# Performance work log

Hardware: AMD Instinct MI355X
Metric: run time of the kernel (lower is better)

The kernel has to match this reference:

```python
import jax, jax.numpy as jnp
import numpy as np

B, S, D, H, DH = 2, 2048, 1024, 16, 64
SCALE = float(np.sqrt(DH))
IGNORE = -100000.0


def setup_inputs() -> dict:
    key = jax.random.key(0)
    ks = jax.random.split(key, 9)
    s = 0.02
    return {
        "x": jax.random.normal(ks[0], (B, S, D), dtype=jnp.float32),
        "W_Q": jax.random.normal(ks[1], (H, DH, D), dtype=jnp.float32) * s,
        "W_K": jax.random.normal(ks[2], (H, DH, D), dtype=jnp.float32) * s,
        "W_V": jax.random.normal(ks[3], (H, DH, D), dtype=jnp.float32) * s,
        "W_O": jax.random.normal(ks[4], (H, D, DH), dtype=jnp.float32) * s,
        "b_Q": jax.random.normal(ks[5], (H, DH), dtype=jnp.float32) * s,
        "b_K": jax.random.normal(ks[6], (H, DH), dtype=jnp.float32) * s,
        "b_V": jax.random.normal(ks[7], (H, DH), dtype=jnp.float32) * s,
        "b_O": jax.random.normal(ks[8], (D,), dtype=jnp.float32) * s,
        "mask": jnp.tril(jnp.ones((S, S), dtype=bool)),  # causal, global attn_type
    }


def reference(x, W_Q, W_K, W_V, W_O, b_Q, b_K, b_V, b_O, mask):
    # q,k,v: [batch, pos, head, d_head]
    q = jnp.einsum('ihm,bpm->bpih', W_Q, x) + b_Q
    k = jnp.einsum('ihm,bpm->bpih', W_K, x) + b_K
    v = jnp.einsum('ihm,bpm->bpih', W_V, x) + b_V
    # scores: [batch, head, q_pos, k_pos]
    attn_scores = jnp.einsum('bpih,bqih->bipq', q, k) / SCALE
    attn_scores = jnp.where(mask, attn_scores, IGNORE)
    attn = jax.nn.softmax(attn_scores, axis=-1)
    # z: [batch, q_pos, head, d_head]
    z = jnp.einsum('bpih,biqp->bqih', v, attn)
    out = jnp.einsum('idh,bqih->bqd', W_O, z) + b_O
    return out
```

## Files before the change

### kernel.cpp

```cpp
#include <hip/hip_runtime.h>
#include <stdint.h>

typedef __attribute__((ext_vector_type(8))) short bf16x8;
typedef __attribute__((ext_vector_type(4))) float f32x4;
typedef __attribute__((ext_vector_type(16))) float f32x16;
typedef __attribute__((ext_vector_type(4))) unsigned short us4;

#define LOG2E 1.44269504088896340736f

__device__ __forceinline__ unsigned short f2bf(float f) {
    union { float f; unsigned u; } v; v.f = f;
    unsigned r = v.u + 0x7FFFu + ((v.u >> 16) & 1u);
    return (unsigned short)(r >> 16);
}
__device__ __forceinline__ float bf2f(unsigned short u) {
    return __uint_as_float(((unsigned)u) << 16);
}

__device__ __forceinline__ unsigned cvtpk(float lo, float hi) {
    unsigned r;
    asm("v_cvt_pk_bf16_f32 %0, %1, %2" : "=v"(r) : "v"(lo), "v"(hi));
    return r;
}
__device__ __forceinline__ void plswap(unsigned &a, unsigned &b) {
    asm volatile("v_permlane32_swap_b32 %0, %1" : "+v"(a), "+v"(b));
}

__device__ __forceinline__ void gld16(const void* g, void* l) {
    __builtin_amdgcn_global_load_lds((const __attribute__((address_space(1))) void*)g,
                                     (__attribute__((address_space(3))) void*)l, 16, 0, 0);
}

__global__ void k_cvt_all(
    const float* __restrict__ x,  const float* __restrict__ WQ,
    const float* __restrict__ WK, const float* __restrict__ WV,
    const float* __restrict__ WO,
    unsigned short* __restrict__ xb,  unsigned short* __restrict__ wqb,
    unsigned short* __restrict__ wkb, unsigned short* __restrict__ wvb,
    unsigned short* __restrict__ wob)
{
    const int blk = blockIdx.x;
    if (blk < 7168) {
        const float* in; unsigned short* out; int base;
        if (blk < 4096)      { in = x;  out = xb;  base = blk; }
        else if (blk < 5120) { in = WQ; out = wqb; base = blk - 4096; }
        else if (blk < 6144) { in = WK; out = wkb; base = blk - 5120; }
        else                 { in = WV; out = wvb; base = blk - 6144; }
        int i = base * 256 + threadIdx.x;
        float4 v = ((const float4*)in)[i];
        us4 o; o.x = f2bf(v.x); o.y = f2bf(v.y); o.z = f2bf(v.z); o.w = f2bf(v.w);
        *(us4*)(out + (size_t)i * 4) = o;
    } else {
        int t = (blk - 7168) * 256 + threadIdx.x;
        int d = t >> 10, nn = t & 1023, i = nn >> 6, h = nn & 63;
        wob[t] = f2bf(WO[(((size_t)i << 10) + d) * 64 + h]);
    }
}

__global__ __launch_bounds__(256) void k_gemm_qkv(
    const unsigned short* __restrict__ Xb,
    const unsigned short* __restrict__ Wq, const unsigned short* __restrict__ Wk,
    const unsigned short* __restrict__ Wv,
    const float* __restrict__ bQ, const float* __restrict__ bK, const float* __restrict__ bV,
    unsigned short* __restrict__ Qb, unsigned short* __restrict__ Kb, unsigned short* __restrict__ VTb)
{
    __shared__ unsigned short As[128][128];
    __shared__ unsigned short Bs[64][128];
    const int which = blockIdx.z;
    const unsigned short* Wp = which == 0 ? Wq : (which == 1 ? Wk : Wv);
    const int bm = blockIdx.x, bn = blockIdx.y;
    const int t = threadIdx.x, lane = t & 63, w = t >> 6;
    const int l15 = lane & 15, l4 = lane >> 4;
    const int rsw = l15 & 7;
    const int c0 = w * 64 + lane;
    const int arow = bm << 7, brow = bn << 6;
    f32x4 acc[2][4] = {};

    for (int k0 = 0; k0 < 1024; k0 += 128) {
        #pragma unroll
        for (int it = 0; it < 8; ++it) {
            int c = it * 256 + c0;
            int row = c >> 4, sl = (c & 15) ^ (row & 7);
            gld16(Xb + ((size_t)(arow + row)) * 1024 + k0 + sl * 8, (char*)As + (c << 4));
        }
        #pragma unroll
        for (int it = 0; it < 4; ++it) {
            int c = it * 256 + c0;
            int row = c >> 4, sl = (c & 15) ^ (row & 7);
            gld16(Wp + ((size_t)(brow + row)) * 1024 + k0 + sl * 8, (char*)Bs + (c << 4));
        }
        __syncthreads();
        const char* Ab = (const char*)As;
        const char* Bb = (const char*)Bs;
        #pragma unroll
        for (int kk = 0; kk < 4; ++kk) {
            bf16x8 af[2], bfg[4];
            #pragma unroll
            for (int m = 0; m < 2; ++m)
                af[m] = *(const bf16x8*)(Ab + (w * 32 + m * 16 + l15) * 256 + (((kk * 4 + l4) ^ rsw) << 4));
            #pragma unroll
            for (int n = 0; n < 4; ++n)
                bfg[n] = *(const bf16x8*)(Bb + (n * 16 + l15) * 256 + (((kk * 4 + l4) ^ rsw) << 4));
            __builtin_amdgcn_s_setprio(1);
            #pragma unroll
            for (int m = 0; m < 2; ++m)
                #pragma unroll
                for (int n = 0; n < 4; ++n)
                    acc[m][n] = __builtin_amdgcn_mfma_f32_16x16x32_bf16(af[m], bfg[n], acc[m][n], 0, 0, 0);
            __builtin_amdgcn_s_setprio(0);
        }
        __syncthreads();
    }
    #pragma unroll
    for (int m = 0; m < 2; ++m) {
        #pragma unroll
        for (int n = 0; n < 4; ++n) {
            int col = (bn << 6) + n * 16 + l15;
            int i = col >> 6, h = col & 63;
            float bias = which == 0 ? bQ[col] : (which == 1 ? bK[col] : bV[col]);
            #pragma unroll
            for (int r = 0; r < 4; ++r) {
                int p = (bm << 7) + w * 32 + m * 16 + (l4 << 2) + r;
                int b = p >> 11, s = p & 2047;
                float v = acc[m][n][r] + bias;
                if (which == 0)
                    Qb[(((((size_t)b << 4) + i) << 11) + s) * 64 + h] = f2bf(v * (0.125f * LOG2E));
                else if (which == 1)
                    Kb[(((((size_t)b << 4) + i) << 11) + s) * 64 + h] = f2bf(v);
                else
                    VTb[(((((size_t)b << 4) + i) << 6) + h) * 2048 + s] = f2bf(v);
            }
        }
    }
}

__global__ __launch_bounds__(128) void k_attn(
    const unsigned short* __restrict__ Qb, const unsigned short* __restrict__ Kb,
    const unsigned short* __restrict__ VTb,
    unsigned short* __restrict__ Zp, float* __restrict__ Lse)
{
    __shared__ __align__(16) char Lbuf[16384];
    const int id = (int)blockIdx.x;
    const int bi = id & 31;
    const int r = id >> 5;
    const int c = 31 - (r >> 1);
    const int part = r & 1;
    const int n = c + 1, n0 = (n + 1) >> 1;
    const int t0 = part ? n0 : 0, t1 = part ? n : n0;
    const int lane = threadIdx.x & 63, w = threadIdx.x >> 6;
    const int l31 = lane & 31, hi = lane >> 5;
    const unsigned short* Qh = Qb + (size_t)bi * 2048 * 64;
    const char* Khb = (const char*)(Kb + (size_t)bi * 2048 * 64);
    const char* Vhb = (const char*)(VTb + (size_t)bi * 64 * 2048);
    const int q0 = c * 64 + w * 32;
    const int q = q0 + l31;

    bf16x8 qf[4];
    #pragma unroll
    for (int kk = 0; kk < 4; ++kk)
        qf[kk] = *(const bf16x8*)&Qh[(size_t)q * 64 + kk * 16 + hi * 8];

    const int r8 = lane >> 3;
    const int swz = ((lane & 7) * 16) ^ (r8 << 4);
    const int koff = r8 * 128 + swz;
    const int voff = r8 * 4096 + swz;

    const int rsw = (l31 & 7) << 4;
    int kaddr[8];
    #pragma unroll
    for (int i = 0; i < 8; ++i)
        kaddr[i] = (l31 + 32 * (i >> 2)) * 128 + ((32 * (i & 3) + 16 * hi) ^ rsw);
    int vcol[4];
    #pragma unroll
    for (int f = 0; f < 4; ++f)
        vcol[f] = ((f * 32 + 16 * hi) ^ rsw);

    f32x16 za0 = {}, za1 = {};
    float m_run = -1e30f, l_run = 0.f;

    if (t0 < t1) {
        if (w == 0) {
            const char* src = Khb + (size_t)t0 * 8192 + koff;
            #pragma unroll
            for (int it = 0; it < 8; ++it) gld16(src + it * 1024, &Lbuf[0] + it * 1024);
        } else {
            const char* src = Vhb + (size_t)t0 * 128 + voff;
            #pragma unroll
            for (int it = 0; it < 8; ++it) gld16(src + it * 32768, &Lbuf[8192] + it * 1024);
        }
    }

    for (int t = t0; t < t1; ++t) {
        __syncthreads();
        const char* KL = &Lbuf[0];
        const char* VL = &Lbuf[8192];
        bf16x8 ka[8];
        #pragma unroll
        for (int i = 0; i < 8; ++i) ka[i] = *(const bf16x8*)(KL + kaddr[i]);
        bf16x8 vf0[4], vf1[4];
        #pragma unroll
        for (int f = 0; f < 4; ++f) {
            vf0[f] = *(const bf16x8*)(VL + l31 * 128 + vcol[f]);
            vf1[f] = *(const bf16x8*)(VL + (l31 + 32) * 128 + vcol[f]);
        }
        __syncthreads();
        if (t + 1 < t1) {
            if (w == 0) {
                const char* src = Khb + (size_t)(t + 1) * 8192 + koff;
                #pragma unroll
                for (int it = 0; it < 8; ++it) gld16(src + it * 1024, &Lbuf[0] + it * 1024);
            } else {
                const char* src = Vhb + (size_t)(t + 1) * 128 + voff;
                #pragma unroll
                for (int it = 0; it < 8; ++it) gld16(src + it * 32768, &Lbuf[8192] + it * 1024);
            }
        }

        const bool full = !(t == c && w == 0);
        f32x16 s0 = {}, s1;
        __builtin_amdgcn_s_setprio(1);
        #pragma unroll
        for (int kk = 0; kk < 4; ++kk)
            s0 = __builtin_amdgcn_mfma_f32_32x32x16_bf16(ka[kk], qf[kk], s0, 0, 0, 0);
        if (full) {
            f32x16 z = {};
            #pragma unroll
            for (int kk = 0; kk < 4; ++kk)
                z = __builtin_amdgcn_mfma_f32_32x32x16_bf16(ka[4 + kk], qf[kk], z, 0, 0, 0);
            s1 = z;
        }
        __builtin_amdgcn_s_setprio(0);

        if (!full) {
            #pragma unroll
            for (int j = 0; j < 16; ++j) s1[j] = -100000.0f;
        }
        if (t == c) {
            #pragma unroll
            for (int j = 0; j < 16; ++j) {
                int kv0 = (j & 3) + 8 * (j >> 2) + 4 * hi;
                if (c * 64 + kv0 > q) s0[j] = -100000.0f;
                if (c * 64 + kv0 + 32 > q) s1[j] = -100000.0f;
            }
        }
        float tmax = -1e30f;
        #pragma unroll
        for (int j = 0; j < 16; ++j) tmax = fmaxf(tmax, fmaxf(s0[j], s1[j]));
        tmax = fmaxf(tmax, __shfl_xor(tmax, 32, 64));
        if (!__all(tmax <= m_run + 8.0f)) {
            float newm = fmaxf(m_run, tmax);
            float alpha = exp2f(m_run - newm);
            m_run = newm;
            l_run *= alpha;
            za0 *= alpha; za1 *= alpha;
        }
        float rsum = 0.f;
        #pragma unroll
        for (int j = 0; j < 16; ++j) { s0[j] = exp2f(s0[j] - m_run); rsum += s0[j]; }
        if (full) {
            #pragma unroll
            for (int j = 0; j < 16; ++j) { s1[j] = exp2f(s1[j] - m_run); rsum += s1[j]; }
        }
        rsum += __shfl_xor(rsum, 32, 64);
        l_run += rsum;

        union { unsigned u[4]; bf16x8 v; } pk0, pk1, pk2, pk3;
        {
            unsigned a0 = cvtpk(s0[0], s0[1]),  a1 = cvtpk(s0[2], s0[3]);
            unsigned a2 = cvtpk(s0[4], s0[5]),  a3 = cvtpk(s0[6], s0[7]);
            plswap(a0, a2); plswap(a1, a3);
            pk0.u[0] = a0; pk0.u[1] = a1; pk0.u[2] = a2; pk0.u[3] = a3;
            unsigned b0 = cvtpk(s0[8], s0[9]),  b1 = cvtpk(s0[10], s0[11]);
            unsigned b2 = cvtpk(s0[12], s0[13]), b3 = cvtpk(s0[14], s0[15]);
            plswap(b0, b2); plswap(b1, b3);
            pk1.u[0] = b0; pk1.u[1] = b1; pk1.u[2] = b2; pk1.u[3] = b3;
        }
        if (full) {
            unsigned a0 = cvtpk(s1[0], s1[1]),  a1 = cvtpk(s1[2], s1[3]);
            unsigned a2 = cvtpk(s1[4], s1[5]),  a3 = cvtpk(s1[6], s1[7]);
            plswap(a0, a2); plswap(a1, a3);
            pk2.u[0] = a0; pk2.u[1] = a1; pk2.u[2] = a2; pk2.u[3] = a3;
            unsigned b0 = cvtpk(s1[8], s1[9]),  b1 = cvtpk(s1[10], s1[11]);
            unsigned b2 = cvtpk(s1[12], s1[13]), b3 = cvtpk(s1[14], s1[15]);
            plswap(b0, b2); plswap(b1, b3);
            pk3.u[0] = b0; pk3.u[1] = b1; pk3.u[2] = b2; pk3.u[3] = b3;
        }
        __builtin_amdgcn_s_setprio(1);
        za0 = __builtin_amdgcn_mfma_f32_32x32x16_bf16(vf0[0], pk0.v, za0, 0, 0, 0);
        za1 = __builtin_amdgcn_mfma_f32_32x32x16_bf16(vf1[0], pk0.v, za1, 0, 0, 0);
        za0 = __builtin_amdgcn_mfma_f32_32x32x16_bf16(vf0[1], pk1.v, za0, 0, 0, 0);
        za1 = __builtin_amdgcn_mfma_f32_32x32x16_bf16(vf1[1], pk1.v, za1, 0, 0, 0);
        if (full) {
            za0 = __builtin_amdgcn_mfma_f32_32x32x16_bf16(vf0[2], pk2.v, za0, 0, 0, 0);
            za1 = __builtin_amdgcn_mfma_f32_32x32x16_bf16(vf1[2], pk2.v, za1, 0, 0, 0);
            za0 = __builtin_amdgcn_mfma_f32_32x32x16_bf16(vf0[3], pk3.v, za0, 0, 0, 0);
            za1 = __builtin_amdgcn_mfma_f32_32x32x16_bf16(vf1[3], pk3.v, za1, 0, 0, 0);
        }
        __builtin_amdgcn_s_setprio(0);
    }

    const float rl = (l_run > 0.f) ? 1.0f / l_run : 0.f;
    const float lse = (l_run > 0.f) ? m_run + log2f(l_run) : -1e30f;
    const int pb = (part << 5) + bi;
    unsigned short* zp = Zp + ((size_t)pb * 2048 + q) * 64;
    #pragma unroll
    for (int nn = 0; nn < 2; ++nn) {
        #pragma unroll
        for (int gg = 0; gg < 4; ++gg) {
            int dh0 = nn * 32 + 8 * gg + 4 * hi;
            us4 o;
            float v0 = (nn ? za1[4 * gg + 0] : za0[4 * gg + 0]) * rl;
            float v1 = (nn ? za1[4 * gg + 1] : za0[4 * gg + 1]) * rl;
            float v2 = (nn ? za1[4 * gg + 2] : za0[4 * gg + 2]) * rl;
            float v3 = (nn ? za1[4 * gg + 3] : za0[4 * gg + 3]) * rl;
            o.x = f2bf(v0); o.y = f2bf(v1); o.z = f2bf(v2); o.w = f2bf(v3);
            *(us4*)(zp + dh0) = o;
        }
    }
    if (hi == 0) Lse[(size_t)pb * 2048 + q] = lse;
}

__global__ __launch_bounds__(256) void k_combine(
    const unsigned short* __restrict__ Zp, const float* __restrict__ Lse,
    unsigned short* __restrict__ Zb)
{
    const int tid = blockIdx.x * 256 + threadIdx.x;
    const int dc = tid & 7, q = (tid >> 3) & 2047, bi = tid >> 14;
    const float l0 = Lse[(size_t)bi * 2048 + q];
    const float l1 = Lse[(size_t)(32 + bi) * 2048 + q];
    const float M = fmaxf(l0, l1);
    float e0 = exp2f(l0 - M), e1 = exp2f(l1 - M);
    const float rs = 1.0f / (e0 + e1);
    e0 *= rs; e1 *= rs;
    const size_t base = ((size_t)bi * 2048 + q) * 64 + dc * 8;
    bf16x8 z0 = *(const bf16x8*)(Zp + base);
    bf16x8 z1 = *(const bf16x8*)(Zp + (size_t)32 * 2048 * 64 + base);
    const int b = bi >> 4, ih = bi & 15;
    unsigned short* op = Zb + (((size_t)b * 2048 + q) << 10) + ih * 64 + dc * 8;
    bf16x8 o;
    #pragma unroll
    for (int j = 0; j < 8; ++j) {
        float v = e0 * bf2f((unsigned short)z0[j]) + e1 * bf2f((unsigned short)z1[j]);
        o[j] = (short)f2bf(v);
    }
    *(bf16x8*)op = o;
}

__global__ __launch_bounds__(256) void k_gemm_out(
    const unsigned short* __restrict__ Zb, const unsigned short* __restrict__ Wo,
    const float* __restrict__ bO, float* __restrict__ out)
{
    __shared__ unsigned short As[128][128];
    __shared__ unsigned short Bs[64][128];
    const int bm = blockIdx.x, bn = blockIdx.y;
    const int t = threadIdx.x, lane = t & 63, w = t >> 6;
    const int l15 = lane & 15, l4 = lane >> 4;
    const int rsw = l15 & 7;
    const int c0 = w * 64 + lane;
    const int arow = bm << 7, brow = bn << 6;
    f32x4 acc[2][4] = {};

    for (int k0 = 0; k0 < 1024; k0 += 128) {
        #pragma unroll
        for (int it = 0; it < 8; ++it) {
            int c = it * 256 + c0;
            int row = c >> 4, sl = (c & 15) ^ (row & 7);
            gld16(Zb + ((size_t)(arow + row)) * 1024 + k0 + sl * 8, (char*)As + (c << 4));
        }
        #pragma unroll
        for (int it = 0; it < 4; ++it) {
            int c = it * 256 + c0;
            int row = c >> 4, sl = (c & 15) ^ (row & 7);
            gld16(Wo + ((size_t)(brow + row)) * 1024 + k0 + sl * 8, (char*)Bs + (c << 4));
        }
        __syncthreads();
        const char* Ab = (const char*)As;
        const char* Bb = (const char*)Bs;
        #pragma unroll
        for (int kk = 0; kk < 4; ++kk) {
            bf16x8 af[2], bfg[4];
            #pragma unroll
            for (int m = 0; m < 2; ++m)
                af[m] = *(const bf16x8*)(Ab + (w * 32 + m * 16 + l15) * 256 + (((kk * 4 + l4) ^ rsw) << 4));
            #pragma unroll
            for (int n = 0; n < 4; ++n)
                bfg[n] = *(const bf16x8*)(Bb + (n * 16 + l15) * 256 + (((kk * 4 + l4) ^ rsw) << 4));
            __builtin_amdgcn_s_setprio(1);
            #pragma unroll
            for (int m = 0; m < 2; ++m)
                #pragma unroll
                for (int n = 0; n < 4; ++n)
                    acc[m][n] = __builtin_amdgcn_mfma_f32_16x16x32_bf16(af[m], bfg[n], acc[m][n], 0, 0, 0);
            __builtin_amdgcn_s_setprio(0);
        }
        __syncthreads();
    }
    #pragma unroll
    for (int m = 0; m < 2; ++m) {
        #pragma unroll
        for (int n = 0; n < 4; ++n) {
            int col = (bn << 6) + n * 16 + l15;
            float bias = bO[col];
            #pragma unroll
            for (int r = 0; r < 4; ++r) {
                int p = (bm << 7) + w * 32 + m * 16 + (l4 << 2) + r;
                out[(size_t)p * 1024 + col] = acc[m][n][r] + bias;
            }
        }
    }
}

extern "C" void kernel_launch(void* const* d_in, const int* in_sizes, int n_in,
                              void* d_out, int out_size, void* d_ws, size_t ws_size,
                              hipStream_t stream)
{
    const float* x  = (const float*)d_in[0];
    const float* WQ = (const float*)d_in[1];
    const float* WK = (const float*)d_in[2];
    const float* WV = (const float*)d_in[3];
    const float* WO = (const float*)d_in[4];
    const float* bQ = (const float*)d_in[5];
    const float* bK = (const float*)d_in[6];
    const float* bV = (const float*)d_in[7];
    const float* bO = (const float*)d_in[8];
    float* out = (float*)d_out;

    char* w = (char*)d_ws;
    unsigned short* xb  = (unsigned short*)w; w += (size_t)4096 * 1024 * 2;
    unsigned short* wqb = (unsigned short*)w; w += (size_t)1024 * 1024 * 2;
    unsigned short* wkb = (unsigned short*)w; w += (size_t)1024 * 1024 * 2;
    unsigned short* wvb = (unsigned short*)w; w += (size_t)1024 * 1024 * 2;
    unsigned short* wob = (unsigned short*)w; w += (size_t)1024 * 1024 * 2;
    unsigned short* Qb  = (unsigned short*)w; w += (size_t)4096 * 1024 * 2;
    unsigned short* Kb  = (unsigned short*)w; w += (size_t)4096 * 1024 * 2;
    unsigned short* VTb = (unsigned short*)w; w += (size_t)4096 * 1024 * 2;
    unsigned short* Zb  = (unsigned short*)w; w += (size_t)4096 * 1024 * 2;
    unsigned short* Zp  = (unsigned short*)w; w += (size_t)2 * 32 * 2048 * 64 * 2;
    float*          Lse = (float*)w;          w += (size_t)2 * 32 * 2048 * 4;

    k_cvt_all<<<11264, 256, 0, stream>>>(x, WQ, WK, WV, WO, xb, wqb, wkb, wvb, wob);

    k_gemm_qkv<<<dim3(32, 16, 3), 256, 0, stream>>>(xb, wqb, wkb, wvb, bQ, bK, bV, Qb, Kb, VTb);
    k_attn<<<2048, 128, 0, stream>>>(Qb, Kb, VTb, Zp, Lse);
    k_combine<<<2048, 256, 0, stream>>>(Zp, Lse, Zb);
    k_gemm_out<<<dim3(32, 16), 256, 0, stream>>>(Zb, wob, bO, out);
}
```

Before: 125.5 us.

## Process two 32-query sub-blocks per wave to double K/V tile reuse

Each attention workgroup now handles 128 query rows: each wave owns two 32-row query sub-blocks, with separate accumulators and softmax state for each. This replaces the previous 64 rows per workgroup, and the grid shrinks from 2048 to 1024 workgroups. The key range is split evenly in two for the two partial-sum parts, and waves skip tiles beyond their causal diagonal. The aim is to halve LDS staging and global K/V traffic per query and to amortise barriers. The costs are higher register pressure, fewer workgroups, and idle waves on diagonal tiles.

```diff
diff --git a/kernel.cpp b/kernel.cpp
--- a/kernel.cpp
+++ b/kernel.cpp
@@ -142,23 +142,25 @@
     __shared__ __align__(16) char Lbuf[16384];
     const int id = (int)blockIdx.x;
     const int bi = id & 31;
-    const int r = id >> 5;
-    const int c = 31 - (r >> 1);
-    const int part = r & 1;
-    const int n = c + 1, n0 = (n + 1) >> 1;
-    const int t0 = part ? n0 : 0, t1 = part ? n : n0;
+    const int rr = id >> 5;
+    const int g = 15 - (rr >> 1);
+    const int part = rr & 1;
+    const int t0 = part * (g + 1), t1 = t0 + g + 1;
     const int lane = threadIdx.x & 63, w = threadIdx.x >> 6;
     const int l31 = lane & 31, hi = lane >> 5;
     const unsigned short* Qh = Qb + (size_t)bi * 2048 * 64;
     const char* Khb = (const char*)(Kb + (size_t)bi * 2048 * 64);
     const char* Vhb = (const char*)(VTb + (size_t)bi * 64 * 2048);
-    const int q0 = c * 64 + w * 32;
-    const int q = q0 + l31;
-
-    bf16x8 qf[4];
-    #pragma unroll
-    for (int kk = 0; kk < 4; ++kk)
-        qf[kk] = *(const bf16x8*)&Qh[(size_t)q * 64 + kk * 16 + hi * 8];
+    const int qA = g * 128 + w * 64 + l31;
+    const int qB = qA + 32;
+    const int dq = 2 * g + w;
+
+    bf16x8 qfA[4], qfB[4];
+    #pragma unroll
+    for (int kk = 0; kk < 4; ++kk) {
+        qfA[kk] = *(const bf16x8*)&Qh[(size_t)qA * 64 + kk * 16 + hi * 8];
+        qfB[kk] = *(const bf16x8*)&Qh[(size_t)qB * 64 + kk * 16 + hi * 8];
+    }
 
     const int r8 = lane >> 3;
     const int swz = ((lane & 7) * 16) ^ (r8 << 4);
@@ -175,33 +177,33 @@
     for (int f = 0; f < 4; ++f)
         vcol[f] = ((f * 32 + 16 * hi) ^ rsw);
 
-    f32x16 za0 = {}, za1 = {};
-    float m_run = -1e30f, l_run = 0.f;
-
-    if (t0 < t1) {
-        if (w == 0) {
-            const char* src = Khb + (size_t)t0 * 8192 + koff;
-            #pragma unroll
-            for (int it = 0; it < 8; ++it) gld16(src + it * 1024, &Lbuf[0] + it * 1024);
-        } else {
-            const char* src = Vhb + (size_t)t0 * 128 + voff;
-            #pragma unroll
-            for (int it = 0; it < 8; ++it) gld16(src + it * 32768, &Lbuf[8192] + it * 1024);
-        }
+    f32x16 zaA0 = {}, zaA1 = {}, zaB0 = {}, zaB1 = {};
+    float mA = -1e30f, lA = 0.f, mB = -1e30f, lB = 0.f;
+
+    if (w == 0) {
+        const char* src = Khb + (size_t)t0 * 8192 + koff;
+        #pragma unroll
+        for (int it = 0; it < 8; ++it) gld16(src + it * 1024, &Lbuf[0] + it * 1024);
+    } else {
+        const char* src = Vhb + (size_t)t0 * 128 + voff;
+        #pragma unroll
+        for (int it = 0; it < 8; ++it) gld16(src + it * 32768, &Lbuf[8192] + it * 1024);
     }
 
     for (int t = t0; t < t1; ++t) {
-        __syncthreads();
-        const char* KL = &Lbuf[0];
-        const char* VL = &Lbuf[8192];
-        bf16x8 ka[8];
-        #pragma unroll
-        for (int i = 0; i < 8; ++i) ka[i] = *(const bf16x8*)(KL + kaddr[i]);
-        bf16x8 vf0[4], vf1[4];
-        #pragma unroll
-        for (int f = 0; f < 4; ++f) {
-            vf0[f] = *(const bf16x8*)(VL + l31 * 128 + vcol[f]);
-            vf1[f] = *(const bf16x8*)(VL + (l31 + 32) * 128 + vcol[f]);
+        const bool active = (t <= dq);
+        __syncthreads();
+        bf16x8 ka[8], vf0[4], vf1[4];
+        if (active) {
+            const char* KL = &Lbuf[0];
+            const char* VL = &Lbuf[8192];
+            #pragma unroll
+            for (int i = 0; i < 8; ++i) ka[i] = *(const bf16x8*)(KL + kaddr[i]);
+            #pragma unroll
+            for (int f = 0; f < 4; ++f) {
+                vf0[f] = *(const bf16x8*)(VL + l31 * 128 + vcol[f]);
+                vf1[f] = *(const bf16x8*)(VL + (l31 + 32) * 128 + vcol[f]);
+            }
         }
         __syncthreads();
         if (t + 1 < t1) {
@@ -215,109 +217,120 @@
                 for (int it = 0; it < 8; ++it) gld16(src + it * 32768, &Lbuf[8192] + it * 1024);
             }
         }
-
-        const bool full = !(t == c && w == 0);
-        f32x16 s0 = {}, s1;
-        __builtin_amdgcn_s_setprio(1);
-        #pragma unroll
-        for (int kk = 0; kk < 4; ++kk)
-            s0 = __builtin_amdgcn_mfma_f32_32x32x16_bf16(ka[kk], qf[kk], s0, 0, 0, 0);
-        if (full) {
-            f32x16 z = {};
-            #pragma unroll
-            for (int kk = 0; kk < 4; ++kk)
-                z = __builtin_amdgcn_mfma_f32_32x32x16_bf16(ka[4 + kk], qf[kk], z, 0, 0, 0);
-            s1 = z;
-        }
-        __builtin_amdgcn_s_setprio(0);
-
-        if (!full) {
-            #pragma unroll
-            for (int j = 0; j < 16; ++j) s1[j] = -100000.0f;
-        }
-        if (t == c) {
-            #pragma unroll
-            for (int j = 0; j < 16; ++j) {
-                int kv0 = (j & 3) + 8 * (j >> 2) + 4 * hi;
-                if (c * 64 + kv0 > q) s0[j] = -100000.0f;
-                if (c * 64 + kv0 + 32 > q) s1[j] = -100000.0f;
-            }
-        }
-        float tmax = -1e30f;
-        #pragma unroll
-        for (int j = 0; j < 16; ++j) tmax = fmaxf(tmax, fmaxf(s0[j], s1[j]));
-        tmax = fmaxf(tmax, __shfl_xor(tmax, 32, 64));
-        if (!__all(tmax <= m_run + 8.0f)) {
-            float newm = fmaxf(m_run, tmax);
-            float alpha = exp2f(m_run - newm);
-            m_run = newm;
-            l_run *= alpha;
-            za0 *= alpha; za1 *= alpha;
-        }
-        float rsum = 0.f;
-        #pragma unroll
-        for (int j = 0; j < 16; ++j) { s0[j] = exp2f(s0[j] - m_run); rsum += s0[j]; }
-        if (full) {
-            #pragma unroll
-            for (int j = 0; j < 16; ++j) { s1[j] = exp2f(s1[j] - m_run); rsum += s1[j]; }
-        }
-        rsum += __shfl_xor(rsum, 32, 64);
-        l_run += rsum;
-
-        union { unsigned u[4]; bf16x8 v; } pk0, pk1, pk2, pk3;
-        {
-            unsigned a0 = cvtpk(s0[0], s0[1]),  a1 = cvtpk(s0[2], s0[3]);
-            unsigned a2 = cvtpk(s0[4], s0[5]),  a3 = cvtpk(s0[6], s0[7]);
-            plswap(a0, a2); plswap(a1, a3);
-            pk0.u[0] = a0; pk0.u[1] = a1; pk0.u[2] = a2; pk0.u[3] = a3;
-            unsigned b0 = cvtpk(s0[8], s0[9]),  b1 = cvtpk(s0[10], s0[11]);
-            unsigned b2 = cvtpk(s0[12], s0[13]), b3 = cvtpk(s0[14], s0[15]);
-            plswap(b0, b2); plswap(b1, b3);
-            pk1.u[0] = b0; pk1.u[1] = b1; pk1.u[2] = b2; pk1.u[3] = b3;
-        }
-        if (full) {
-            unsigned a0 = cvtpk(s1[0], s1[1]),  a1 = cvtpk(s1[2], s1[3]);
-            unsigned a2 = cvtpk(s1[4], s1[5]),  a3 = cvtpk(s1[6], s1[7]);
-            plswap(a0, a2); plswap(a1, a3);
-            pk2.u[0] = a0; pk2.u[1] = a1; pk2.u[2] = a2; pk2.u[3] = a3;
-            unsigned b0 = cvtpk(s1[8], s1[9]),  b1 = cvtpk(s1[10], s1[11]);
-            unsigned b2 = cvtpk(s1[12], s1[13]), b3 = cvtpk(s1[14], s1[15]);
-            plswap(b0, b2); plswap(b1, b3);
-            pk3.u[0] = b0; pk3.u[1] = b1; pk3.u[2] = b2; pk3.u[3] = b3;
-        }
-        __builtin_amdgcn_s_setprio(1);
-        za0 = __builtin_amdgcn_mfma_f32_32x32x16_bf16(vf0[0], pk0.v, za0, 0, 0, 0);
-        za1 = __builtin_amdgcn_mfma_f32_32x32x16_bf16(vf1[0], pk0.v, za1, 0, 0, 0);
-        za0 = __builtin_amdgcn_mfma_f32_32x32x16_bf16(vf0[1], pk1.v, za0, 0, 0, 0);
-        za1 = __builtin_amdgcn_mfma_f32_32x32x16_bf16(vf1[1], pk1.v, za1, 0, 0, 0);
-        if (full) {
-            za0 = __builtin_amdgcn_mfma_f32_32x32x16_bf16(vf0[2], pk2.v, za0, 0, 0, 0);
-            za1 = __builtin_amdgcn_mfma_f32_32x32x16_bf16(vf1[2], pk2.v, za1, 0, 0, 0);
-            za0 = __builtin_amdgcn_mfma_f32_32x32x16_bf16(vf0[3], pk3.v, za0, 0, 0, 0);
-            za1 = __builtin_amdgcn_mfma_f32_32x32x16_bf16(vf1[3], pk3.v, za1, 0, 0, 0);
-        }
-        __builtin_amdgcn_s_setprio(0);
-    }
-
-    const float rl = (l_run > 0.f) ? 1.0f / l_run : 0.f;
-    const float lse = (l_run > 0.f) ? m_run + log2f(l_run) : -1e30f;
+        if (!active) continue;
+
+#define ATTN_SUB(QX, QFX, ZX0, ZX1, MX, LX, ISLOWER)                              \
+        {                                                                         \
+            const bool full = !(t == dq && (ISLOWER));                            \
+            f32x16 s0 = {}, s1;                                                   \
+            __builtin_amdgcn_s_setprio(1);                                        \
+            _Pragma("unroll")                                                     \
+            for (int kk = 0; kk < 4; ++kk)                                        \
+                s0 = __builtin_amdgcn_mfma_f32_32x32x16_bf16(ka[kk], QFX[kk], s0, 0, 0, 0); \
+            if (full) {                                                           \
+                f32x16 z = {};                                                    \
+                _Pragma("unroll")                                                 \
+                for (int kk = 0; kk < 4; ++kk)                                    \
+                    z = __builtin_amdgcn_mfma_f32_32x32x16_bf16(ka[4 + kk], QFX[kk], z, 0, 0, 0); \
+                s1 = z;                                                           \
+            }                                                                     \
+            __builtin_amdgcn_s_setprio(0);                                        \
+            if (!full) {                                                          \
+                _Pragma("unroll")                                                 \
+                for (int j = 0; j < 16; ++j) s1[j] = -100000.0f;                  \
+            }                                                                     \
+            if (t == dq) {                                                        \
+                _Pragma("unroll")                                                 \
+                for (int j = 0; j < 16; ++j) {                                    \
+                    int kv0 = (j & 3) + 8 * (j >> 2) + 4 * hi;                    \
+                    if (t * 64 + kv0 > (QX)) s0[j] = -100000.0f;                  \
+                    if (t * 64 + kv0 + 32 > (QX)) s1[j] = -100000.0f;             \
+                }                                                                 \
+            }                                                                     \
+            float tmax = -1e30f;                                                  \
+            _Pragma("unroll")                                                     \
+            for (int j = 0; j < 16; ++j) tmax = fmaxf(tmax, fmaxf(s0[j], s1[j])); \
+            tmax = fmaxf(tmax, __shfl_xor(tmax, 32, 64));                         \
+            if (!__all(tmax <= (MX) + 8.0f)) {                                    \
+                float newm = fmaxf((MX), tmax);                                   \
+                float alpha = exp2f((MX) - newm);                                 \
+                (MX) = newm;                                                      \
+                (LX) *= alpha;                                                    \
+                ZX0 *= alpha; ZX1 *= alpha;                                       \
+            }                                                                     \
+            float rsum = 0.f;                                                     \
+            _Pragma("unroll")                                                     \
+            for (int j = 0; j < 16; ++j) { s0[j] = exp2f(s0[j] - (MX)); rsum += s0[j]; } \
+            if (full) {                                                           \
+                _Pragma("unroll")                                                 \
+                for (int j = 0; j < 16; ++j) { s1[j] = exp2f(s1[j] - (MX)); rsum += s1[j]; } \
+            }                                                                     \
+            rsum += __shfl_xor(rsum, 32, 64);                                     \
+            (LX) += rsum;                                                         \
+            union { unsigned u[4]; bf16x8 v; } pk0, pk1, pk2, pk3;                \
+            {                                                                     \
+                unsigned a0 = cvtpk(s0[0], s0[1]),  a1 = cvtpk(s0[2], s0[3]);     \
+                unsigned a2 = cvtpk(s0[4], s0[5]),  a3 = cvtpk(s0[6], s0[7]);     \
+                plswap(a0, a2); plswap(a1, a3);                                   \
+                pk0.u[0] = a0; pk0.u[1] = a1; pk0.u[2] = a2; pk0.u[3] = a3;       \
+                unsigned b0 = cvtpk(s0[8], s0[9]),  b1 = cvtpk(s0[10], s0[11]);   \
+                unsigned b2 = cvtpk(s0[12], s0[13]), b3 = cvtpk(s0[14], s0[15]);  \
+                plswap(b0, b2); plswap(b1, b3);                                   \
+                pk1.u[0] = b0; pk1.u[1] = b1; pk1.u[2] = b2; pk1.u[3] = b3;       \
+            }                                                                     \
+            if (full) {                                                           \
+                unsigned a0 = cvtpk(s1[0], s1[1]),  a1 = cvtpk(s1[2], s1[3]);     \
+                unsigned a2 = cvtpk(s1[4], s1[5]),  a3 = cvtpk(s1[6], s1[7]);     \
+                plswap(a0, a2); plswap(a1, a3);                                   \
+                pk2.u[0] = a0; pk2.u[1] = a1; pk2.u[2] = a2; pk2.u[3] = a3;       \
+                unsigned b0 = cvtpk(s1[8], s1[9]),  b1 = cvtpk(s1[10], s1[11]);   \
+                unsigned b2 = cvtpk(s1[12], s1[13]), b3 = cvtpk(s1[14], s1[15]);  \
+                plswap(b0, b2); plswap(b1, b3);                                   \
+                pk3.u[0] = b0; pk3.u[1] = b1; pk3.u[2] = b2; pk3.u[3] = b3;       \
+            }                                                                     \
+            __builtin_amdgcn_s_setprio(1);                                        \
+            ZX0 = __builtin_amdgcn_mfma_f32_32x32x16_bf16(vf0[0], pk0.v, ZX0, 0, 0, 0); \
+            ZX1 = __builtin_amdgcn_mfma_f32_32x32x16_bf16(vf1[0], pk0.v, ZX1, 0, 0, 0); \
+            ZX0 = __builtin_amdgcn_mfma_f32_32x32x16_bf16(vf0[1], pk1.v, ZX0, 0, 0, 0); \
+            ZX1 = __builtin_amdgcn_mfma_f32_32x32x16_bf16(vf1[1], pk1.v, ZX1, 0, 0, 0); \
+            if (full) {                                                           \
+                ZX0 = __builtin_amdgcn_mfma_f32_32x32x16_bf16(vf0[2], pk2.v, ZX0, 0, 0, 0); \
+                ZX1 = __builtin_amdgcn_mfma_f32_32x32x16_bf16(vf1[2], pk2.v, ZX1, 0, 0, 0); \
+                ZX0 = __builtin_amdgcn_mfma_f32_32x32x16_bf16(vf0[3], pk3.v, ZX0, 0, 0, 0); \
+                ZX1 = __builtin_amdgcn_mfma_f32_32x32x16_bf16(vf1[3], pk3.v, ZX1, 0, 0, 0); \
+            }                                                                     \
+            __builtin_amdgcn_s_setprio(0);                                        \
+        }
+        ATTN_SUB(qA, qfA, zaA0, zaA1, mA, lA, true)
+        ATTN_SUB(qB, qfB, zaB0, zaB1, mB, lB, false)
+#undef ATTN_SUB
+    }
+
     const int pb = (part << 5) + bi;
-    unsigned short* zp = Zp + ((size_t)pb * 2048 + q) * 64;
-    #pragma unroll
-    for (int nn = 0; nn < 2; ++nn) {
-        #pragma unroll
-        for (int gg = 0; gg < 4; ++gg) {
-            int dh0 = nn * 32 + 8 * gg + 4 * hi;
-            us4 o;
-            float v0 = (nn ? za1[4 * gg + 0] : za0[4 * gg + 0]) * rl;
-            float v1 = (nn ? za1[4 * gg + 1] : za0[4 * gg + 1]) * rl;
-            float v2 = (nn ? za1[4 * gg + 2] : za0[4 * gg + 2]) * rl;
-            float v3 = (nn ? za1[4 * gg + 3] : za0[4 * gg + 3]) * rl;
-            o.x = f2bf(v0); o.y = f2bf(v1); o.z = f2bf(v2); o.w = f2bf(v3);
-            *(us4*)(zp + dh0) = o;
-        }
-    }
-    if (hi == 0) Lse[(size_t)pb * 2048 + q] = lse;
+#define ATTN_EPI(QX, ZX0, ZX1, MX, LX)                                            \
+    {                                                                             \
+        const float rl = ((LX) > 0.f) ? 1.0f / (LX) : 0.f;                        \
+        const float lse = ((LX) > 0.f) ? (MX) + log2f((LX)) : -1e30f;             \
+        unsigned short* zp = Zp + ((size_t)pb * 2048 + (QX)) * 64;                \
+        _Pragma("unroll")                                                         \
+        for (int nn = 0; nn < 2; ++nn) {                                          \
+            _Pragma("unroll")                                                     \
+            for (int gg = 0; gg < 4; ++gg) {                                      \
+                int dh0 = nn * 32 + 8 * gg + 4 * hi;                              \
+                us4 o;                                                            \
+                float v0 = (nn ? ZX1[4 * gg + 0] : ZX0[4 * gg + 0]) * rl;         \
+                float v1 = (nn ? ZX1[4 * gg + 1] : ZX0[4 * gg + 1]) * rl;         \
+                float v2 = (nn ? ZX1[4 * gg + 2] : ZX0[4 * gg + 2]) * rl;         \
+                float v3 = (nn ? ZX1[4 * gg + 3] : ZX0[4 * gg + 3]) * rl;         \
+                o.x = f2bf(v0); o.y = f2bf(v1); o.z = f2bf(v2); o.w = f2bf(v3);   \
+                *(us4*)(zp + dh0) = o;                                            \
+            }                                                                     \
+        }                                                                         \
+        if (hi == 0) Lse[(size_t)pb * 2048 + (QX)] = lse;                         \
+    }
+    ATTN_EPI(qA, zaA0, zaA1, mA, lA)
+    ATTN_EPI(qB, zaB0, zaB1, mB, lB)
+#undef ATTN_EPI
 }
 
 __global__ __launch_bounds__(256) void k_combine(
@@ -441,7 +454,7 @@
     k_cvt_all<<<11264, 256, 0, stream>>>(x, WQ, WK, WV, WO, xb, wqb, wkb, wvb, wob);
 
     k_gemm_qkv<<<dim3(32, 16, 3), 256, 0, stream>>>(xb, wqb, wkb, wvb, bQ, bK, bV, Qb, Kb, VTb);
-    k_attn<<<2048, 128, 0, stream>>>(Qb, Kb, VTb, Zp, Lse);
+    k_attn<<<1024, 128, 0, stream>>>(Qb, Kb, VTb, Zp, Lse);
     k_combine<<<2048, 256, 0, stream>>>(Zp, Lse, Zb);
     k_gemm_out<<<dim3(32, 16), 256, 0, stream>>>(Zb, wob, bO, out);
 }
```

Measured after the change: 135.4 us. 7.9% more time.

## Double-buffer K/V tiles and process two tiles per barrier pair in attention

Applied to the files above, without the earlier changes.

Doubles the LDS staging buffer so two consecutive K/V tiles are resident, and restructures the attention loop to handle two tiles per iteration with one pair of barriers. The second tile's fragments are read into registers before the barrier, which lets the next two tiles' global-to-LDS loads overlap with the second body's compute. This halves barrier count and lengthens the prefetch distance, at the cost of more LDS and extra registers for a second fragment set, which may reduce occupancy.

```diff
diff --git a/kernel.cpp b/kernel.cpp
--- a/kernel.cpp
+++ b/kernel.cpp
@@ -139,7 +139,7 @@
     const unsigned short* __restrict__ VTb,
     unsigned short* __restrict__ Zp, float* __restrict__ Lse)
 {
-    __shared__ __align__(16) char Lbuf[16384];
+    __shared__ __align__(16) char Lbuf[32768];
     const int id = (int)blockIdx.x;
     const int bi = id & 31;
     const int r = id >> 5;
@@ -178,126 +178,132 @@
     f32x16 za0 = {}, za1 = {};
     float m_run = -1e30f, l_run = 0.f;
 
+#define STAGE_T(TT, HALF)                                                         \
+    if (w == 0) {                                                                 \
+        const char* src_ = Khb + (size_t)(TT) * 8192 + koff;                      \
+        _Pragma("unroll")                                                         \
+        for (int it = 0; it < 8; ++it) gld16(src_ + it * 1024, &Lbuf[(HALF) * 16384] + it * 1024); \
+    } else {                                                                      \
+        const char* src_ = Vhb + (size_t)(TT) * 128 + voff;                       \
+        _Pragma("unroll")                                                         \
+        for (int it = 0; it < 8; ++it) gld16(src_ + it * 32768, &Lbuf[(HALF) * 16384 + 8192] + it * 1024); \
+    }
+
+#define READ_FRAGS(KL, VL, KA, V0, V1)                                            \
+    {                                                                             \
+        _Pragma("unroll")                                                         \
+        for (int i = 0; i < 8; ++i) KA[i] = *(const bf16x8*)((KL) + kaddr[i]);    \
+        _Pragma("unroll")                                                         \
+        for (int f = 0; f < 4; ++f) {                                             \
+            V0[f] = *(const bf16x8*)((VL) + l31 * 128 + vcol[f]);                 \
+            V1[f] = *(const bf16x8*)((VL) + (l31 + 32) * 128 + vcol[f]);          \
+        }                                                                         \
+    }
+
+#define BODY(T, KA, V0, V1)                                                       \
+    {                                                                             \
+        const bool full = !((T) == c && w == 0);                                  \
+        f32x16 s0 = {}, s1;                                                       \
+        __builtin_amdgcn_s_setprio(1);                                            \
+        _Pragma("unroll")                                                         \
+        for (int kk = 0; kk < 4; ++kk)                                            \
+            s0 = __builtin_amdgcn_mfma_f32_32x32x16_bf16(KA[kk], qf[kk], s0, 0, 0, 0); \
+        if (full) {                                                               \
+            f32x16 z = {};                                                        \
+            _Pragma("unroll")                                                     \
+            for (int kk = 0; kk < 4; ++kk)                                        \
+                z = __builtin_amdgcn_mfma_f32_32x32x16_bf16(KA[4 + kk], qf[kk], z, 0, 0, 0); \
+            s1 = z;                                                               \
+        }                                                                         \
+        __builtin_amdgcn_s_setprio(0);                                            \
+        if (!full) {                                                              \
+            _Pragma("unroll")                                                     \
+            for (int j = 0; j < 16; ++j) s1[j] = -100000.0f;                      \
+        }                                                                         \
+        if ((T) == c) {                                                           \
+            _Pragma("unroll")                                                     \
+            for (int j = 0; j < 16; ++j) {                                        \
+                int kv0 = (j & 3) + 8 * (j >> 2) + 4 * hi;                        \
+                if ((T) * 64 + kv0 > q) s0[j] = -100000.0f;                       \
+                if ((T) * 64 + kv0 + 32 > q) s1[j] = -100000.0f;                  \
+            }                                                                     \
+        }                                                                         \
+        float tmax = -1e30f;                                                      \
+        _Pragma("unroll")                                                         \
+        for (int j = 0; j < 16; ++j) tmax = fmaxf(tmax, fmaxf(s0[j], s1[j]));     \
+        tmax = fmaxf(tmax, __shfl_xor(tmax, 32, 64));                             \
+        if (!__all(tmax <= m_run + 8.0f)) {                                       \
+            float newm = fmaxf(m_run, tmax);                                      \
+            float alpha = exp2f(m_run - newm);                                    \
+            m_run = newm;                                                         \
+            l_run *= alpha;                                                       \
+            za0 *= alpha; za1 *= alpha;                                           \
+        }                                                                         \
+        float rsum = 0.f;                                                         \
+        _Pragma("unroll")                                                         \
+        for (int j = 0; j < 16; ++j) { s0[j] = exp2f(s0[j] - m_run); rsum += s0[j]; } \
+        if (full) {                                                               \
+            _Pragma("unroll")                                                     \
+            for (int j = 0; j < 16; ++j) { s1[j] = exp2f(s1[j] - m_run); rsum += s1[j]; } \
+        }                                                                         \
+        rsum += __shfl_xor(rsum, 32, 64);                                         \
+        l_run += rsum;                                                            \
+        union { unsigned u[4]; bf16x8 v; } pk0, pk1, pk2, pk3;                    \
+        {                                                                         \
+            unsigned a0 = cvtpk(s0[0], s0[1]),  a1 = cvtpk(s0[2], s0[3]);         \
+            unsigned a2 = cvtpk(s0[4], s0[5]),  a3 = cvtpk(s0[6], s0[7]);         \
+            plswap(a0, a2); plswap(a1, a3);                                       \
+            pk0.u[0] = a0; pk0.u[1] = a1; pk0.u[2] = a2; pk0.u[3] = a3;           \
+            unsigned b0 = cvtpk(s0[8], s0[9]),  b1 = cvtpk(s0[10], s0[11]);       \
+            unsigned b2 = cvtpk(s0[12], s0[13]), b3 = cvtpk(s0[14], s0[15]);      \
+            plswap(b0, b2); plswap(b1, b3);                                       \
+            pk1.u[0] = b0; pk1.u[1] = b1; pk1.u[2] = b2; pk1.u[3] = b3;           \
+        }                                                                         \
+        if (full) {                                                               \
+            unsigned a0 = cvtpk(s1[0], s1[1]),  a1 = cvtpk(s1[2], s1[3]);         \
+            unsigned a2 = cvtpk(s1[4], s1[5]),  a3 = cvtpk(s1[6], s1[7]);         \
+            plswap(a0, a2); plswap(a1, a3);                                       \
+            pk2.u[0] = a0; pk2.u[1] = a1; pk2.u[2] = a2; pk2.u[3] = a3;           \
+            unsigned b0 = cvtpk(s1[8], s1[9]),  b1 = cvtpk(s1[10], s1[11]);       \
+            unsigned b2 = cvtpk(s1[12], s1[13]), b3 = cvtpk(s1[14], s1[15]);      \
+            plswap(b0, b2); plswap(b1, b3);                                       \
+            pk3.u[0] = b0; pk3.u[1] = b1; pk3.u[2] = b2; pk3.u[3] = b3;           \
+        }                                                                         \
+        __builtin_amdgcn_s_setprio(1);                                            \
+        za0 = __builtin_amdgcn_mfma_f32_32x32x16_bf16(V0[0], pk0.v, za0, 0, 0, 0); \
+        za1 = __builtin_amdgcn_mfma_f32_32x32x16_bf16(V1[0], pk0.v, za1, 0, 0, 0); \
+        za0 = __builtin_amdgcn_mfma_f32_32x32x16_bf16(V0[1], pk1.v, za0, 0, 0, 0); \
+        za1 = __builtin_amdgcn_mfma_f32_32x32x16_bf16(V1[1], pk1.v, za1, 0, 0, 0); \
+        if (full) {                                                               \
+            za0 = __builtin_amdgcn_mfma_f32_32x32x16_bf16(V0[2], pk2.v, za0, 0, 0, 0); \
+            za1 = __builtin_amdgcn_mfma_f32_32x32x16_bf16(V1[2], pk2.v, za1, 0, 0, 0); \
+            za0 = __builtin_amdgcn_mfma_f32_32x32x16_bf16(V0[3], pk3.v, za0, 0, 0, 0); \
+            za1 = __builtin_amdgcn_mfma_f32_32x32x16_bf16(V1[3], pk3.v, za1, 0, 0, 0); \
+        }                                                                         \
+        __builtin_amdgcn_s_setprio(0);                                            \
+    }
+
     if (t0 < t1) {
-        if (w == 0) {
-            const char* src = Khb + (size_t)t0 * 8192 + koff;
-            #pragma unroll
-            for (int it = 0; it < 8; ++it) gld16(src + it * 1024, &Lbuf[0] + it * 1024);
-        } else {
-            const char* src = Vhb + (size_t)t0 * 128 + voff;
-            #pragma unroll
-            for (int it = 0; it < 8; ++it) gld16(src + it * 32768, &Lbuf[8192] + it * 1024);
-        }
-    }
-
-    for (int t = t0; t < t1; ++t) {
-        __syncthreads();
-        const char* KL = &Lbuf[0];
-        const char* VL = &Lbuf[8192];
-        bf16x8 ka[8];
-        #pragma unroll
-        for (int i = 0; i < 8; ++i) ka[i] = *(const bf16x8*)(KL + kaddr[i]);
-        bf16x8 vf0[4], vf1[4];
-        #pragma unroll
-        for (int f = 0; f < 4; ++f) {
-            vf0[f] = *(const bf16x8*)(VL + l31 * 128 + vcol[f]);
-            vf1[f] = *(const bf16x8*)(VL + (l31 + 32) * 128 + vcol[f]);
-        }
-        __syncthreads();
-        if (t + 1 < t1) {
-            if (w == 0) {
-                const char* src = Khb + (size_t)(t + 1) * 8192 + koff;
-                #pragma unroll
-                for (int it = 0; it < 8; ++it) gld16(src + it * 1024, &Lbuf[0] + it * 1024);
-            } else {
-                const char* src = Vhb + (size_t)(t + 1) * 128 + voff;
-                #pragma unroll
-                for (int it = 0; it < 8; ++it) gld16(src + it * 32768, &Lbuf[8192] + it * 1024);
-            }
-        }
-
-        const bool full = !(t == c && w == 0);
-        f32x16 s0 = {}, s1;
-        __builtin_amdgcn_s_setprio(1);
-        #pragma unroll
-        for (int kk = 0; kk < 4; ++kk)
-            s0 = __builtin_amdgcn_mfma_f32_32x32x16_bf16(ka[kk], qf[kk], s0, 0, 0, 0);
-        if (full) {
-            f32x16 z = {};
-            #pragma unroll
-            for (int kk = 0; kk < 4; ++kk)
-                z = __builtin_amdgcn_mfma_f32_32x32x16_bf16(ka[4 + kk], qf[kk], z, 0, 0, 0);
-            s1 = z;
-        }
-        __builtin_amdgcn_s_setprio(0);
-
-        if (!full) {
-            #pragma unroll
-            for (int j = 0; j < 16; ++j) s1[j] = -100000.0f;
-        }
-        if (t == c) {
-            #pragma unroll
-            for (int j = 0; j < 16; ++j) {
-                int kv0 = (j & 3) + 8 * (j >> 2) + 4 * hi;
-                if (c * 64 + kv0 > q) s0[j] = -100000.0f;
-                if (c * 64 + kv0 + 32 > q) s1[j] = -100000.0f;
-            }
-        }
-        float tmax = -1e30f;
-        #pragma unroll
-        for (int j = 0; j < 16; ++j) tmax = fmaxf(tmax, fmaxf(s0[j], s1[j]));
-        tmax = fmaxf(tmax, __shfl_xor(tmax, 32, 64));
-        if (!__all(tmax <= m_run + 8.0f)) {
-            float newm = fmaxf(m_run, tmax);
-            float alpha = exp2f(m_run - newm);
-            m_run = newm;
-            l_run *= alpha;
-            za0 *= alpha; za1 *= alpha;
-        }
-        float rsum = 0.f;
-        #pragma unroll
-        for (int j = 0; j < 16; ++j) { s0[j] = exp2f(s0[j] - m_run); rsum += s0[j]; }
-        if (full) {
-            #pragma unroll
-            for (int j = 0; j < 16; ++j) { s1[j] = exp2f(s1[j] - m_run); rsum += s1[j]; }
-        }
-        rsum += __shfl_xor(rsum, 32, 64);
-        l_run += rsum;
-
-        union { unsigned u[4]; bf16x8 v; } pk0, pk1, pk2, pk3;
-        {
-            unsigned a0 = cvtpk(s0[0], s0[1]),  a1 = cvtpk(s0[2], s0[3]);
-            unsigned a2 = cvtpk(s0[4], s0[5]),  a3 = cvtpk(s0[6], s0[7]);
-            plswap(a0, a2); plswap(a1, a3);
-            pk0.u[0] = a0; pk0.u[1] = a1; pk0.u[2] = a2; pk0.u[3] = a3;
-            unsigned b0 = cvtpk(s0[8], s0[9]),  b1 = cvtpk(s0[10], s0[11]);
-            unsigned b2 = cvtpk(s0[12], s0[13]), b3 = cvtpk(s0[14], s0[15]);
-            plswap(b0, b2); plswap(b1, b3);
-            pk1.u[0] = b0; pk1.u[1] = b1; pk1.u[2] = b2; pk1.u[3] = b3;
-        }
-        if (full) {
-            unsigned a0 = cvtpk(s1[0], s1[1]),  a1 = cvtpk(s1[2], s1[3]);
-            unsigned a2 = cvtpk(s1[4], s1[5]),  a3 = cvtpk(s1[6], s1[7]);
-            plswap(a0, a2); plswap(a1, a3);
-            pk2.u[0] = a0; pk2.u[1] = a1; pk2.u[2] = a2; pk2.u[3] = a3;
-            unsigned b0 = cvtpk(s1[8], s1[9]),  b1 = cvtpk(s1[10], s1[11]);
-            unsigned b2 = cvtpk(s1[12], s1[13]), b3 = cvtpk(s1[14], s1[15]);
-            plswap(b0, b2); plswap(b1, b3);
-            pk3.u[0] = b0; pk3.u[1] = b1; pk3.u[2] = b2; pk3.u[3] = b3;
-        }
-        __builtin_amdgcn_s_setprio(1);
-        za0 = __builtin_amdgcn_mfma_f32_32x32x16_bf16(vf0[0], pk0.v, za0, 0, 0, 0);
-        za1 = __builtin_amdgcn_mfma_f32_32x32x16_bf16(vf1[0], pk0.v, za1, 0, 0, 0);
-        za0 = __builtin_amdgcn_mfma_f32_32x32x16_bf16(vf0[1], pk1.v, za0, 0, 0, 0);
-        za1 = __builtin_amdgcn_mfma_f32_32x32x16_bf16(vf1[1], pk1.v, za1, 0, 0, 0);
-        if (full) {
-            za0 = __builtin_amdgcn_mfma_f32_32x32x16_bf16(vf0[2], pk2.v, za0, 0, 0, 0);
-            za1 = __builtin_amdgcn_mfma_f32_32x32x16_bf16(vf1[2], pk2.v, za1, 0, 0, 0);
-            za0 = __builtin_amdgcn_mfma_f32_32x32x16_bf16(vf0[3], pk3.v, za0, 0, 0, 0);
-            za1 = __builtin_amdgcn_mfma_f32_32x32x16_bf16(vf1[3], pk3.v, za1, 0, 0, 0);
-        }
-        __builtin_amdgcn_s_setprio(0);
-    }
+        STAGE_T(t0, 0);
+        if (t0 + 1 < t1) { STAGE_T(t0 + 1, 1); }
+    }
+
+    for (int tb = t0; tb < t1; tb += 2) {
+        const bool hasB = (tb + 1 < t1);
+        __syncthreads();
+        bf16x8 kaA[8], vA0[4], vA1[4];
+        READ_FRAGS(&Lbuf[0], &Lbuf[8192], kaA, vA0, vA1);
+        BODY(tb, kaA, vA0, vA1);
+        bf16x8 kaB[8], vB0[4], vB1[4];
+        if (hasB) READ_FRAGS(&Lbuf[16384], &Lbuf[24576], kaB, vB0, vB1);
+        __syncthreads();
+        if (tb + 2 < t1) { STAGE_T(tb + 2, 0); }
+        if (tb + 3 < t1) { STAGE_T(tb + 3, 1); }
+        if (hasB) BODY(tb + 1, kaB, vB0, vB1);
+    }
+#undef STAGE_T
+#undef READ_FRAGS
+#undef BODY
 
     const float rl = (l_run > 0.f) ? 1.0f / l_run : 0.f;
     const float lse = (l_run > 0.f) ? m_run + log2f(l_run) : -1e30f;
```

Result: slower. 139.7 us (+11.4%).
